# Kernel optimization log

Measured on AMD Instinct MI355X. Metric: run time of the kernel, lower is better.

Reference implementation:

```python
import jax, jax.numpy as jnp
import numpy as np

N_NODES = 20000
N_EDGES = 320000
N_GRAPHS = 64
D = 128  # node_dim


def _gat_conv(h, W, al, ar, b, src, dst, n, res=None, act=None):
    # DGL GATConv: fc -> per-head attn logits -> leaky_relu -> edge softmax per dst -> scatter-add
    H, Dh = al.shape
    feat = (h @ W).reshape(n, H, Dh)                      # [N,H,D]
    el = jnp.einsum('nhd,hd->nh', feat, al)               # [N,H]
    er = jnp.einsum('nhd,hd->nh', feat, ar)               # [N,H]
    e = jax.nn.leaky_relu(el[src] + er[dst], 0.2)         # [E,H]
    m = jax.ops.segment_max(e, dst, num_segments=n)       # [N,H]
    m = jnp.where(jnp.isfinite(m), m, 0.0)
    a = jnp.exp(e - m[dst])                               # [E,H]
    den = jax.ops.segment_sum(a, dst, num_segments=n)     # [N,H]
    a = a / jnp.maximum(den, 1e-9)[dst]
    out = jax.ops.segment_sum(a[:, :, None] * feat[src], dst, num_segments=n)  # [N,H,D]
    if res is not None:
        out = out + res
    out = out + b.reshape(1, H, Dh)
    return act(out) if act is not None else out


def setup_inputs() -> dict:
    key = jax.random.key(0)
    ks = jax.random.split(key, 20)
    s = 0.05
    inp = {
        'h': jax.random.normal(ks[0], (N_NODES, D), jnp.float32),
        'he': jax.random.normal(ks[1], (N_EDGES, 64), jnp.float32),
        'src': jax.random.randint(ks[2], (N_EDGES,), 0, N_NODES),
        'dst': jax.random.randint(ks[3], (N_EDGES,), 0, N_NODES),
        'graph_id': jnp.sort(jax.random.randint(ks[4], (N_NODES,), 0, N_GRAPHS)),
        # layer 0: in=D, heads=4, out=D
        'W0': jax.random.normal(ks[5], (D, 4 * D), jnp.float32) * s,
        'al0': jax.random.normal(ks[6], (4, D), jnp.float32) * s,
        'ar0': jax.random.normal(ks[7], (4, D), jnp.float32) * s,
        'b0': jnp.zeros((4 * D,), jnp.float32),
        # layer 1: in=4D, heads=4, out=D, residual (identity since 4D==4*D)
        'W1': jax.random.normal(ks[8], (4 * D, 4 * D), jnp.float32) * s,
        'al1': jax.random.normal(ks[9], (4, D), jnp.float32) * s,
        'ar1': jax.random.normal(ks[10], (4, D), jnp.float32) * s,
        'b1': jnp.zeros((4 * D,), jnp.float32),
        # layer 2: in=4D, heads=6, out=D, residual via res_fc (4D -> 6D)
        'W2': jax.random.normal(ks[11], (4 * D, 6 * D), jnp.float32) * s,
        'al2': jax.random.normal(ks[12], (6, D), jnp.float32) * s,
        'ar2': jax.random.normal(ks[13], (6, D), jnp.float32) * s,
        'b2': jnp.zeros((6 * D,), jnp.float32),
        'resW2': jax.random.normal(ks[14], (4 * D, 6 * D), jnp.float32) * s,
        # final MLP (1 layer): Linear(D, D)
        'Wm': jax.random.normal(ks[15], (D, D), jnp.float32) * s,
        'bm': jnp.zeros((D,), jnp.float32),
    }
    return inp


def reference(h, he, src, dst, graph_id, W0, al0, ar0, b0, W1, al1, ar1, b1,
              W2, al2, ar2, b2, resW2, Wm, bm):
    n = h.shape[0]
    elu = jax.nn.elu
    # layer 0 (no residual, elu), flatten heads
    x = _gat_conv(h, W0, al0, ar0, b0, src, dst, n, res=None, act=elu)
    x = x.reshape(n, -1)  # [N, 4D]
    # layer 1 (identity residual, elu), flatten heads
    res1 = x.reshape(n, 4, D)
    x2 = _gat_conv(x, W1, al1, ar1, b1, src, dst, n, res=res1, act=elu)
    x2 = x2.reshape(n, -1)  # [N, 4D]
    # layer 2 (linear residual, no activation), mean over heads
    res2 = (x2 @ resW2).reshape(n, 6, D)
    x3 = _gat_conv(x2, W2, al2, ar2, b2, src, dst, n, res=res2, act=None)
    local_feat = x3.mean(axis=1)  # [N, D]
    # avg pooling per graph + linear
    sums = jax.ops.segment_sum(local_feat, graph_id, num_segments=N_GRAPHS)
    cnts = jax.ops.segment_sum(jnp.ones((n,), local_feat.dtype), graph_id, num_segments=N_GRAPHS)
    pooled = sums / jnp.maximum(cnts, 1.0)[:, None]  # [G, D]
    global_feat = pooled @ Wm + bm
    return (local_feat, global_feat)
```

## Files before the change

### kernel.cpp

```cpp
#include <hip/hip_runtime.h>
#include <math.h>


typedef _Float16 f16;
typedef __attribute__((ext_vector_type(8))) _Float16 half8;
typedef __attribute__((ext_vector_type(4))) _Float16 half4;
typedef __attribute__((ext_vector_type(4))) float float4v;

union U16 { unsigned short u; _Float16 h; };

#define M_PAD 20096
#define CHSTRIDE ((size_t)M_PAD * 64)

__device__ inline void gload_lds16(const void* g, void* l) {
    __builtin_amdgcn_global_load_lds((const __attribute__((address_space(1))) unsigned*)g,
                                     (__attribute__((address_space(3))) unsigned*)l,
                                     16, 0, 0);
}


__global__ __launch_bounds__(256) void deg_kernel(const int* __restrict__ dst,
                                                  int* __restrict__ deg, int E) {
    int e = blockIdx.x * 256 + threadIdx.x;
    if (e < E) atomicAdd(&deg[dst[e]], 1);
}

__global__ __launch_bounds__(1024) void scan_kernel(const int* __restrict__ deg,
                                                    int* __restrict__ row_off,
                                                    const int* __restrict__ gid,
                                                    int* __restrict__ gstart, int n) {
    __shared__ int sums[1024];
    int t = threadIdx.x;
    if (t <= 64) {
        int g = t, lo = 0, hi = n;
        while (lo < hi) {
            int mid = (lo + hi) >> 1;
            if (gid[mid] < g) lo = mid + 1; else hi = mid;
        }
        gstart[g] = lo;
    }
    int CH = (n + 1023) >> 10;
    int base = t * CH;
    int s = 0;
    for (int i = 0; i < CH; ++i) { int idx = base + i; if (idx < n) s += deg[idx]; }
    sums[t] = s;
    __syncthreads();
    for (int off = 1; off < 1024; off <<= 1) {
        int v = (t >= off) ? sums[t - off] : 0;
        __syncthreads();
        sums[t] += v;
        __syncthreads();
    }
    int run = (t == 0) ? 0 : sums[t - 1];
    for (int i = 0; i < CH; ++i) {
        int idx = base + i;
        if (idx < n) { row_off[idx] = run; run += deg[idx]; }
    }
    if (t == 1023) row_off[n] = run;
}

__global__ __launch_bounds__(256) void fill_kernel(const int* __restrict__ src,
                                                   const int* __restrict__ dst,
                                                   const int* __restrict__ row_off,
                                                   int* __restrict__ fill,
                                                   int* __restrict__ csr_src, int E) {
    int e = blockIdx.x * 256 + threadIdx.x;
    if (e < E) {
        int d = dst[e];
        int pos = row_off[d] + atomicAdd(&fill[d], 1);
        csr_src[pos] = src[e];
    }
}


__global__ __launch_bounds__(256) void cvt_pad_kernel(const float* __restrict__ x,
                                                      f16* __restrict__ y,
                                                      long n_valid, long n_total) {
    long i = ((long)blockIdx.x * 256 + threadIdx.x) * 4;
    if (i >= n_total) return;
    float4 v = make_float4(0.f, 0.f, 0.f, 0.f);
    if (i < n_valid) v = *(const float4*)&x[i];
    half4 o; o[0] = (f16)v.x; o[1] = (f16)v.y; o[2] = (f16)v.z; o[3] = (f16)v.w;
    *(half4*)&y[i] = o;
}

__global__ __launch_bounds__(256) void zero_pad_kernel(f16* __restrict__ x1,
                                                       f16* __restrict__ x2, int n) {
    int total = (M_PAD - n) * 512;
    int idx = (blockIdx.x * 256 + threadIdx.x) * 4;
    if (idx < total) {
        half4 z; z[0] = (f16)0.f; z[1] = (f16)0.f; z[2] = (f16)0.f; z[3] = (f16)0.f;
        *(half4*)&x1[(size_t)n * 512 + idx] = z;
        *(half4*)&x2[(size_t)n * 512 + idx] = z;
    }
}

__global__ __launch_bounds__(256) void transpose_cvt_kernel(const float* __restrict__ W,
                                                            f16* __restrict__ Wt,
                                                            int K, int N) {
    __shared__ float tile[32][33];
    int n0 = blockIdx.x * 32, k0 = blockIdx.y * 32;
    int tx = threadIdx.x, ty = threadIdx.y;
#pragma unroll
    for (int i = 0; i < 32; i += 8)
        tile[ty + i][tx] = W[(size_t)(k0 + ty + i) * N + n0 + tx];
    __syncthreads();
#pragma unroll
    for (int i = 0; i < 32; i += 8)
        Wt[(size_t)(n0 + ty + i) * K + k0 + tx] = (f16)tile[tx][ty + i];
}


#define STAGE(buf, k0) do {                                   \
    f16* a_ = As + (buf) * 4096 + t * 8;                      \
    f16* b_ = Bs + (buf) * 4096 + t * 8;                      \
    gload_lds16(ag0 + (k0), a_);                              \
    gload_lds16(ag1 + (k0), a_ + 2048);                       \
    gload_lds16(bg0 + (k0), b_);                              \
    gload_lds16(bg1 + (k0), b_ + 2048);                       \
} while (0)

__global__ __launch_bounds__(256) void gemm16_kernel(const f16* __restrict__ A,
                                                     const f16* __restrict__ Bt,
                                                     f16* __restrict__ Cc,
                                                     f16* __restrict__ Cr,
                                                     const float* __restrict__ al,
                                                     const float* __restrict__ ar,
                                                     float* __restrict__ el8,
                                                     float* __restrict__ er8,
                                                     int N, int K, int nchunk,
                                                     int nheads, int nvalid) {
    __shared__ f16 As[2 * 128 * 32];
    __shared__ f16 Bs[2 * 128 * 32];
    __shared__ float elds[2][2][128];
    int t = threadIdx.x;
    int w = t >> 6;
    int l = t & 63;

    int gx = gridDim.x;
    int nwg = gx * gridDim.y;
    int wg = blockIdx.y * gx + blockIdx.x;
    int qq = nwg >> 3, rr = nwg & 7;
    int xcd = wg & 7, idx = wg >> 3;
    int swz = (xcd < rr ? xcd * (qq + 1) : rr * (qq + 1) + (xcd - rr) * qq) + idx;
    int bxi = swz % gx;
    int byi = swz / gx;

    size_t bm = (size_t)byi * 128;
    int bn = bxi * 128;
    int wm = (w & 1) * 64;
    int wn = (w >> 1) * 64;

    int srow = t >> 2;
    int sq = (t & 3) ^ ((srow >> 1) & 3);
    const f16* ag0 = A + (bm + srow) * K + sq * 8;
    const f16* ag1 = A + (bm + 64 + srow) * K + sq * 8;
    const f16* bg0 = Bt + (size_t)(bn + srow) * K + sq * 8;
    const f16* bg1 = Bt + (size_t)(bn + 64 + srow) * K + sq * 8;

    float4v acc[4][4];
#pragma unroll
    for (int i = 0; i < 4; ++i)
#pragma unroll
        for (int j = 0; j < 4; ++j) acc[i][j] = (float4v)(0.f);

    int ml = l & 15, q = l >> 4;
    int sslot = (q ^ ((ml >> 1) & 3)) * 8;
    int apoff = (wm + ml) * 32 + sslot;
    int bpoff = (wn + ml) * 32 + sslot;

    STAGE(0, 0);
    __syncthreads();
    int cur = 0;
    for (int k0 = 0; k0 < K; k0 += 32) {
        if (k0 + 32 < K) STAGE(cur ^ 1, k0 + 32);
        const f16* ap = As + cur * 4096 + apoff;
        const f16* bp = Bs + cur * 4096 + bpoff;
        half8 af[4], bf[4];
#pragma unroll
        for (int mt = 0; mt < 4; ++mt) af[mt] = *(const half8*)(ap + mt * 16 * 32);
#pragma unroll
        for (int nt = 0; nt < 4; ++nt) bf[nt] = *(const half8*)(bp + nt * 16 * 32);
#pragma unroll
        for (int mt = 0; mt < 4; ++mt)
#pragma unroll
            for (int nt = 0; nt < 4; ++nt)
                acc[mt][nt] = __builtin_amdgcn_mfma_f32_16x16x32_f16(bf[nt], af[mt],
                                                                     acc[mt][nt], 0, 0, 0);
        __syncthreads();
        cur ^= 1;
    }
#pragma unroll
    for (int mt = 0; mt < 4; ++mt) {
        size_t row = bm + wm + mt * 16 + ml;
#pragma unroll
        for (int nt = 0; nt < 4; ++nt) {
            half4 hv;
#pragma unroll
            for (int r = 0; r < 4; ++r) hv[r] = (f16)acc[mt][nt][r];
            int col = bn + wn + nt * 16 + q * 4;
            if (col < nchunk) {
                *(half4*)&Cc[(size_t)(col >> 6) * CHSTRIDE + row * 64 + (col & 63)] = hv;
            } else {
                *(half4*)&Cr[row * (size_t)(N - nchunk) + (col - nchunk)] = hv;
            }
        }
    }
    if (al != nullptr && bn < nheads * 128) {
        int hh = bn >> 7;
        float4 a4[4], r4[4];
#pragma unroll
        for (int nt = 0; nt < 4; ++nt) {
            int ci = hh * 128 + wn + nt * 16 + q * 4;
            a4[nt] = *(const float4*)&al[ci];
            r4[nt] = *(const float4*)&ar[ci];
        }
        int wnidx = wn >> 6;
#pragma unroll
        for (int mt = 0; mt < 4; ++mt) {
            float ep = 0.f, rp = 0.f;
#pragma unroll
            for (int nt = 0; nt < 4; ++nt) {
                ep += acc[mt][nt][0] * a4[nt].x + acc[mt][nt][1] * a4[nt].y
                    + acc[mt][nt][2] * a4[nt].z + acc[mt][nt][3] * a4[nt].w;
                rp += acc[mt][nt][0] * r4[nt].x + acc[mt][nt][1] * r4[nt].y
                    + acc[mt][nt][2] * r4[nt].z + acc[mt][nt][3] * r4[nt].w;
            }
            ep += __shfl_xor(ep, 16, 64); ep += __shfl_xor(ep, 32, 64);
            rp += __shfl_xor(rp, 16, 64); rp += __shfl_xor(rp, 32, 64);
            if (q == 0) {
                elds[0][wnidx][wm + mt * 16 + ml] = ep;
                elds[1][wnidx][wm + mt * 16 + ml] = rp;
            }
        }
        __syncthreads();
        int row = t & 127, which = t >> 7;
        long gv = (long)bm + row;
        if (gv < nvalid) {
            float vs = elds[which][0][row] + elds[which][1][row];
            if (which == 0) el8[gv * 8 + hh] = vs;
            else            er8[gv * 8 + hh] = vs;
        }
    }
}


__global__ __launch_bounds__(256, 8) void edge_weight_kernel(
        const float* __restrict__ el8, const float* __restrict__ er8,
        const int* __restrict__ row_off, const int* __restrict__ csr_src,
        unsigned short* __restrict__ wexp, float* __restrict__ inv8,
        int H, int n, int E) {
    int wid = threadIdx.x >> 6, lane = threadIdx.x & 63;
    int c2 = lane >> 4;
    int sl = lane & 15;
    int v = blockIdx.x * 16 + wid * 4 + c2;
    if (v >= n) return;
    float era[6];
    {
        float4 a = *(const float4*)&er8[(size_t)v * 8];
        float2 b = *(const float2*)&er8[(size_t)v * 8 + 4];
        era[0] = a.x; era[1] = a.y; era[2] = a.z; era[3] = a.w;
        era[4] = b.x; era[5] = b.y;
    }
    int beg = row_off[v], end = row_off[v + 1];
    float lsum[6] = {0.f, 0.f, 0.f, 0.f, 0.f, 0.f};
    for (int pos = beg; pos < end; pos += 16) {
        int cnt = min(16, end - pos);
        int s_l = (sl < cnt) ? csr_src[pos + sl] : 0;
        float4 a = *(const float4*)&el8[(size_t)s_l * 8];
        float2 bq = *(const float2*)&el8[(size_t)s_l * 8 + 4];
        float ee[6] = {a.x, a.y, a.z, a.w, bq.x, bq.y};
#pragma unroll
        for (int h = 0; h < 6; ++h) {
            if (h < H) {
                float lg = ee[h] + era[h];
                lg = (lg >= 0.f) ? lg : 0.2f * lg;
                float wv = __expf(lg);
                if (sl >= cnt) wv = 0.f;
                lsum[h] += wv;
                if (sl < cnt) {
                    U16 uu; uu.h = (f16)wv;
                    wexp[(size_t)h * E + pos + sl] = uu.u;
                }
            }
        }
    }
#pragma unroll
    for (int h = 0; h < 6; ++h)
#pragma unroll
        for (int off = 8; off >= 1; off >>= 1)
            lsum[h] += __shfl_xor(lsum[h], off, 64);
    if (sl == 0) {
#pragma unroll
        for (int h = 0; h < 6; ++h)
            if (h < H) inv8[(size_t)v * 8 + h] = 1.f / fmaxf(lsum[h], 1e-9f);
    }
}


__device__ __forceinline__ void agg_chunk_body(
        const f16* __restrict__ fc, const unsigned short* __restrict__ wh,
        const float* __restrict__ inv8, int head,
        const int* __restrict__ row_off, const int* __restrict__ csr_src,
        const f16* __restrict__ res, const float* __restrict__ bias,
        f16* __restrict__ out16, float* __restrict__ out32,
        int n, int width, int act, int chunk,
        int wave_id, int wavestride, int lane) {
    int c = lane >> 3;
    int j = lane & 7;
    int coff = j * 8;
    int cb = chunk * 64 + coff;
    float4 bv0 = *(const float4*)&bias[cb];
    float4 bv1 = *(const float4*)&bias[cb + 4];
    int clbase = lane & 56;

    for (int v0 = wave_id * 8; v0 < n; v0 += wavestride * 8) {
        int v = v0 + c;
        bool valid = (v < n);
        int beg = 0, end = 0;
        if (valid) { beg = row_off[v]; end = row_off[v + 1]; }
        int rounds = end - beg;
        rounds = max(rounds, __shfl_xor(rounds, 8, 64));
        rounds = max(rounds, __shfl_xor(rounds, 16, 64));
        rounds = max(rounds, __shfl_xor(rounds, 32, 64));
        float acc[8] = {0.f, 0.f, 0.f, 0.f, 0.f, 0.f, 0.f, 0.f};
        int s_pf = 0, w_pf = 0;
        for (int r = 0; r < rounds; ++r) {
            if ((r & 7) == 0) {
                int pidx = beg + r + j;
                bool ok = pidx < end;
                s_pf = ok ? csr_src[pidx] : 0;
                w_pf = ok ? (int)wh[pidx] : 0;
            }
            int srcl = clbase + (r & 7);
            int s  = __shfl(s_pf, srcl, 64);
            int wi = __shfl(w_pf, srcl, 64);
            U16 uu; uu.u = (unsigned short)wi;
            float wv = (float)uu.h;
            half8 f = *(const half8*)&fc[(size_t)s * 64 + coff];
#pragma unroll
            for (int k = 0; k < 8; ++k) acc[k] += wv * (float)f[k];
        }
        if (valid) {
            float inv = inv8[(size_t)v * 8 + head];
            float ox[8];
#pragma unroll
            for (int k = 0; k < 8; ++k) ox[k] = acc[k] * inv;
            size_t base = (size_t)v * width + cb;
            if (res) {
                half8 rr = *(const half8*)&res[base];
#pragma unroll
                for (int k = 0; k < 8; ++k) ox[k] += (float)rr[k];
            }
            ox[0] += bv0.x; ox[1] += bv0.y; ox[2] += bv0.z; ox[3] += bv0.w;
            ox[4] += bv1.x; ox[5] += bv1.y; ox[6] += bv1.z; ox[7] += bv1.w;
            if (act) {
#pragma unroll
                for (int k = 0; k < 8; ++k)
                    ox[k] = (ox[k] > 0.f) ? ox[k] : expm1f(ox[k]);
            }
            if (out16) {
                half8 o;
#pragma unroll
                for (int k = 0; k < 8; ++k) o[k] = (f16)ox[k];
                *(half8*)&out16[base] = o;
            } else {
                *(float4*)&out32[base]     = make_float4(ox[0], ox[1], ox[2], ox[3]);
                *(float4*)&out32[base + 4] = make_float4(ox[4], ox[5], ox[6], ox[7]);
            }
        }
    }
}

__global__ __launch_bounds__(256, 8) void agg_chunk_kernel(
        const f16* __restrict__ featc, const unsigned short* __restrict__ wexp,
        const float* __restrict__ inv8,
        const int* __restrict__ row_off, const int* __restrict__ csr_src,
        const f16* __restrict__ res, const float* __restrict__ bias,
        f16* __restrict__ out16, float* __restrict__ out32,
        int n, int nchunks, int width, int E, int act) {
    int wid = threadIdx.x >> 6, lane = threadIdx.x & 63;
    int b = blockIdx.x;
    {
        int chunk = b & 7;
        agg_chunk_body(featc + (size_t)chunk * CHSTRIDE, wexp + (size_t)(chunk >> 1) * E,
                       inv8, chunk >> 1, row_off, csr_src, res, bias, out16, out32,
                       n, width, act, chunk, (b >> 3) * 4 + wid, 1024, lane);
    }
    if (nchunks > 8) {
        int chunk = 8 + (b & 3);
        if (chunk < nchunks)
            agg_chunk_body(featc + (size_t)chunk * CHSTRIDE, wexp + (size_t)(chunk >> 1) * E,
                           inv8, chunk >> 1, row_off, csr_src, res, bias, out16, out32,
                           n, width, act, chunk, (b >> 2) * 4 + wid, 2048, lane);
    }
}


__global__ __launch_bounds__(128) void mean_pool_kernel(const float* __restrict__ x3,
                                                        float* __restrict__ local, int n) {
    int v = blockIdx.x;
    int d = threadIdx.x;
    const float* p = x3 + (size_t)v * 768;
    float s = 0.f;
#pragma unroll
    for (int h = 0; h < 6; ++h) s += p[h * 128 + d];
    local[(size_t)v * 128 + d] = s * (1.f / 6.f);
}

__global__ __launch_bounds__(256) void graph_pool_kernel(const float* __restrict__ local,
                                                         const int* __restrict__ gstart,
                                                         float* __restrict__ pooled) {
    __shared__ float buf[128];
    int g = blockIdx.x;
    int t = threadIdx.x;
    int c = t & 127;
    int sub = t >> 7;
    int beg = gstart[g], end = gstart[g + 1];
    float s = 0.f;
    for (int v = beg + sub; v < end; v += 2) s += local[(size_t)v * 128 + c];
    if (sub == 1) buf[c] = s;
    __syncthreads();
    if (sub == 0) {
        float tot = s + buf[c];
        float cntf = fmaxf((float)(end - beg), 1.f);
        pooled[g * 128 + c] = tot / cntf;
    }
}

__global__ void final_mlp_kernel(const float* __restrict__ pooled,
                                 const float* __restrict__ Wm,
                                 const float* __restrict__ bm,
                                 float* __restrict__ gout) {
    int g = blockIdx.x;
    int j = threadIdx.x;
    __shared__ float p[128];
    p[j] = pooled[g * 128 + j];
    __syncthreads();
    float s = 0.f;
#pragma unroll 16
    for (int k = 0; k < 128; ++k) s += p[k] * Wm[k * 128 + j];
    gout[g * 128 + j] = s + bm[j];
}


extern "C" void kernel_launch(void* const* d_in, const int* in_sizes, int n_in,
                              void* d_out, int out_size, void* d_ws, size_t ws_size,
                              hipStream_t stream) {
    const float* h     = (const float*)d_in[0];
    const int*   src   = (const int*)d_in[2];
    const int*   dst   = (const int*)d_in[3];
    const int*   gid   = (const int*)d_in[4];
    const float* W0    = (const float*)d_in[5];
    const float* al0   = (const float*)d_in[6];
    const float* ar0   = (const float*)d_in[7];
    const float* b0    = (const float*)d_in[8];
    const float* W1    = (const float*)d_in[9];
    const float* al1   = (const float*)d_in[10];
    const float* ar1   = (const float*)d_in[11];
    const float* b1    = (const float*)d_in[12];
    const float* W2    = (const float*)d_in[13];
    const float* al2   = (const float*)d_in[14];
    const float* ar2   = (const float*)d_in[15];
    const float* b2    = (const float*)d_in[16];
    const float* resW2 = (const float*)d_in[17];
    const float* Wm    = (const float*)d_in[18];
    const float* bm    = (const float*)d_in[19];

    const int n = in_sizes[0] / 128;
    const int E = in_sizes[2];

    size_t off = 0;
    auto take = [&](size_t bytes) -> void* {
        void* p = (char*)d_ws + off;
        off = (off + bytes + 255) & ~(size_t)255;
        return p;
    };
    f16* h16     = (f16*)take((size_t)M_PAD * 128 * 2);
    f16* Wt0     = (f16*)take((size_t)512 * 128 * 2);
    f16* Wt1     = (f16*)take((size_t)512 * 512 * 2);
    f16* Wt2cat  = (f16*)take((size_t)1536 * 512 * 2);
    f16* featc   = (f16*)take((size_t)12 * CHSTRIDE * 2);
    f16* res2    = (f16*)take((size_t)M_PAD * 768 * 2);
    f16* x1_16   = (f16*)take((size_t)M_PAD * 512 * 2);
    f16* x2_16   = (f16*)take((size_t)M_PAD * 512 * 2);
    float* x3    = (float*)take((size_t)n * 768 * 4);
    unsigned short* wexp = (unsigned short*)take((size_t)6 * E * 2);
    float* inv8  = (float*)take((size_t)n * 8 * 4);
    float* el8   = (float*)take((size_t)n * 8 * 4);
    float* er8   = (float*)take((size_t)n * 8 * 4);
    int* deg     = (int*)take((size_t)2 * n * 4);
    int* fillc   = deg + n;
    int* row_off = (int*)take((size_t)(n + 1) * 4);
    int* csr_src = (int*)take((size_t)E * 4);
    int* gstart  = (int*)take(65 * 4);
    float* pooled = (float*)take(64 * 128 * 4);

    float* out_local  = (float*)d_out;
    float* out_global = (float*)d_out + (size_t)n * 128;

    hipMemsetAsync(deg, 0, (size_t)2 * n * 4, stream);
    zero_pad_kernel<<<(int)(((size_t)(M_PAD - n) * 512 / 4 + 255) / 256), 256, 0, stream>>>(x1_16, x2_16, n);

    {
        long nv = (long)n * 128, nt = (long)M_PAD * 128;
        cvt_pad_kernel<<<(int)((nt / 4 + 255) / 256), 256, 0, stream>>>(h, h16, nv, nt);
    }
    transpose_cvt_kernel<<<dim3(512 / 32, 128 / 32), dim3(32, 8), 0, stream>>>(W0, Wt0, 128, 512);
    transpose_cvt_kernel<<<dim3(512 / 32, 512 / 32), dim3(32, 8), 0, stream>>>(W1, Wt1, 512, 512);
    transpose_cvt_kernel<<<dim3(768 / 32, 512 / 32), dim3(32, 8), 0, stream>>>(W2, Wt2cat, 512, 768);
    transpose_cvt_kernel<<<dim3(768 / 32, 512 / 32), dim3(32, 8), 0, stream>>>(resW2, Wt2cat + (size_t)768 * 512, 512, 768);

    deg_kernel<<<(E + 255) / 256, 256, 0, stream>>>(dst, deg, E);
    scan_kernel<<<1, 1024, 0, stream>>>(deg, row_off, gid, gstart, n);
    fill_kernel<<<(E + 255) / 256, 256, 0, stream>>>(src, dst, row_off, fillc, csr_src, E);

    const int gy = M_PAD / 128;
    const int ew_blocks = (n + 15) / 16;

    gemm16_kernel<<<dim3(512 / 128, gy), 256, 0, stream>>>(h16, Wt0, featc, nullptr,
                                                           al0, ar0, el8, er8, 512, 128, 512, 4, n);
    edge_weight_kernel<<<ew_blocks, 256, 0, stream>>>(el8, er8, row_off, csr_src, wexp, inv8, 4, n, E);
    agg_chunk_kernel<<<2048, 256, 0, stream>>>(featc, wexp, inv8, row_off, csr_src,
                                               nullptr, b0, x1_16, nullptr, n, 8, 512, E, 1);
    gemm16_kernel<<<dim3(512 / 128, gy), 256, 0, stream>>>(x1_16, Wt1, featc, nullptr,
                                                           al1, ar1, el8, er8, 512, 512, 512, 4, n);
    edge_weight_kernel<<<ew_blocks, 256, 0, stream>>>(el8, er8, row_off, csr_src, wexp, inv8, 4, n, E);
    agg_chunk_kernel<<<2048, 256, 0, stream>>>(featc, wexp, inv8, row_off, csr_src,
                                               x1_16, b1, x2_16, nullptr, n, 8, 512, E, 1);
    gemm16_kernel<<<dim3(1536 / 128, gy), 256, 0, stream>>>(x2_16, Wt2cat, featc, res2,
                                                            al2, ar2, el8, er8, 1536, 512, 768, 6, n);
    edge_weight_kernel<<<ew_blocks, 256, 0, stream>>>(el8, er8, row_off, csr_src, wexp, inv8, 6, n, E);
    agg_chunk_kernel<<<2048, 256, 0, stream>>>(featc, wexp, inv8, row_off, csr_src,
                                               res2, b2, nullptr, x3, n, 12, 768, E, 0);
    mean_pool_kernel<<<n, 128, 0, stream>>>(x3, out_local, n);
    graph_pool_kernel<<<64, 256, 0, stream>>>(out_local, gstart, pooled);
    final_mlp_kernel<<<64, 128, 0, stream>>>(pooled, Wm, bm, out_global);
}
```

Measured before the change: 555.5 us.

## Pack src index with fp16 weight, batch gathers, fuse head-mean and pooling

The edge-weight kernel now writes a packed 32-bit word holding the source index (low 16 bits) and the fp16 attention weight (high 16 bits), so aggregation reads one stream instead of two. The aggregation loop issues eight feature gathers per round with the next packed words prefetched, aiming to raise memory-level parallelism; launch bounds drop to 5 waves per SIMD to fit the extra registers. The last layer adds the head mean straight into the output with float atomics, which removes the x3 buffer and the mean kernel, and graph pooling is fused with the final linear layer. The risks are atomic contention plus a non-deterministic summation order, and the 16-bit index packing, which only holds while the node count stays below 65536.

```diff
diff --git a/kernel.cpp b/kernel.cpp
--- a/kernel.cpp
+++ b/kernel.cpp
@@ -248,7 +248,7 @@
 __global__ __launch_bounds__(256, 8) void edge_weight_kernel(
         const float* __restrict__ el8, const float* __restrict__ er8,
         const int* __restrict__ row_off, const int* __restrict__ csr_src,
-        unsigned short* __restrict__ wexp, float* __restrict__ inv8,
+        int* __restrict__ wp, float* __restrict__ inv8,
         int H, int n, int E) {
     int wid = threadIdx.x >> 6, lane = threadIdx.x & 63;
     int c2 = lane >> 4;
@@ -280,7 +280,7 @@
                 lsum[h] += wv;
                 if (sl < cnt) {
                     U16 uu; uu.h = (f16)wv;
-                    wexp[(size_t)h * E + pos + sl] = uu.u;
+                    wp[(size_t)h * E + pos + sl] = s_l | ((int)uu.u << 16);
                 }
             }
         }
@@ -299,12 +299,12 @@
 
 
 __device__ __forceinline__ void agg_chunk_body(
-        const f16* __restrict__ fc, const unsigned short* __restrict__ wh,
+        const f16* __restrict__ fc, const int* __restrict__ wp,
         const float* __restrict__ inv8, int head,
-        const int* __restrict__ row_off, const int* __restrict__ csr_src,
+        const int* __restrict__ row_off,
         const f16* __restrict__ res, const float* __restrict__ bias,
         f16* __restrict__ out16, float* __restrict__ out32,
-        int n, int width, int act, int chunk,
+        int n, int width, int act, int domean, int chunk,
         int wave_id, int wavestride, int lane) {
     int c = lane >> 3;
     int j = lane & 7;
@@ -324,22 +324,26 @@
         rounds = max(rounds, __shfl_xor(rounds, 16, 64));
         rounds = max(rounds, __shfl_xor(rounds, 32, 64));
         float acc[8] = {0.f, 0.f, 0.f, 0.f, 0.f, 0.f, 0.f, 0.f};
-        int s_pf = 0, w_pf = 0;
-        for (int r = 0; r < rounds; ++r) {
-            if ((r & 7) == 0) {
-                int pidx = beg + r + j;
-                bool ok = pidx < end;
-                s_pf = ok ? csr_src[pidx] : 0;
-                w_pf = ok ? (int)wh[pidx] : 0;
-            }
-            int srcl = clbase + (r & 7);
-            int s  = __shfl(s_pf, srcl, 64);
-            int wi = __shfl(w_pf, srcl, 64);
-            U16 uu; uu.u = (unsigned short)wi;
-            float wv = (float)uu.h;
-            half8 f = *(const half8*)&fc[(size_t)s * 64 + coff];
-#pragma unroll
-            for (int k = 0; k < 8; ++k) acc[k] += wv * (float)f[k];
+        int pidx = beg + j;
+        int pk = (pidx < end) ? wp[pidx] : 0;
+        for (int base = 0; base < rounds; base += 8) {
+            int pn = beg + base + 8 + j;
+            int pk_nxt = (pn < end) ? wp[pn] : 0;
+            int pe[8];
+#pragma unroll
+            for (int e = 0; e < 8; ++e) pe[e] = __shfl(pk, clbase + e, 64);
+            half8 f[8];
+#pragma unroll
+            for (int e = 0; e < 8; ++e)
+                f[e] = *(const half8*)&fc[(size_t)(pe[e] & 0xFFFF) * 64 + coff];
+#pragma unroll
+            for (int e = 0; e < 8; ++e) {
+                U16 uu; uu.u = (unsigned short)((unsigned)pe[e] >> 16);
+                float wv = (float)uu.h;
+#pragma unroll
+                for (int k = 0; k < 8; ++k) acc[k] += wv * (float)f[e][k];
+            }
+            pk = pk_nxt;
         }
         if (valid) {
             float inv = inv8[(size_t)v * 8 + head];
@@ -359,7 +363,11 @@
                 for (int k = 0; k < 8; ++k)
                     ox[k] = (ox[k] > 0.f) ? ox[k] : expm1f(ox[k]);
             }
-            if (out16) {
+            if (domean) {
+                float* dst = out32 + (size_t)v * 128 + (cb & 127);
+#pragma unroll
+                for (int k = 0; k < 8; ++k) atomicAdd(&dst[k], ox[k] * (1.f / 6.f));
+            } else if (out16) {
                 half8 o;
 #pragma unroll
                 for (int k = 0; k < 8; ++k) o[k] = (f16)ox[k];
@@ -372,75 +380,61 @@
     }
 }
 
-__global__ __launch_bounds__(256, 8) void agg_chunk_kernel(
-        const f16* __restrict__ featc, const unsigned short* __restrict__ wexp,
+__global__ __launch_bounds__(256, 5) void agg_chunk_kernel(
+        const f16* __restrict__ featc, const int* __restrict__ wp,
         const float* __restrict__ inv8,
-        const int* __restrict__ row_off, const int* __restrict__ csr_src,
+        const int* __restrict__ row_off,
         const f16* __restrict__ res, const float* __restrict__ bias,
         f16* __restrict__ out16, float* __restrict__ out32,
-        int n, int nchunks, int width, int E, int act) {
+        int n, int nchunks, int width, int E, int act, int domean) {
     int wid = threadIdx.x >> 6, lane = threadIdx.x & 63;
     int b = blockIdx.x;
     {
         int chunk = b & 7;
-        agg_chunk_body(featc + (size_t)chunk * CHSTRIDE, wexp + (size_t)(chunk >> 1) * E,
-                       inv8, chunk >> 1, row_off, csr_src, res, bias, out16, out32,
-                       n, width, act, chunk, (b >> 3) * 4 + wid, 1024, lane);
+        agg_chunk_body(featc + (size_t)chunk * CHSTRIDE, wp + (size_t)(chunk >> 1) * E,
+                       inv8, chunk >> 1, row_off, res, bias, out16, out32,
+                       n, width, act, domean, chunk, (b >> 3) * 4 + wid, 1024, lane);
     }
     if (nchunks > 8) {
         int chunk = 8 + (b & 3);
         if (chunk < nchunks)
-            agg_chunk_body(featc + (size_t)chunk * CHSTRIDE, wexp + (size_t)(chunk >> 1) * E,
-                           inv8, chunk >> 1, row_off, csr_src, res, bias, out16, out32,
-                           n, width, act, chunk, (b >> 2) * 4 + wid, 2048, lane);
-    }
-}
-
-
-__global__ __launch_bounds__(128) void mean_pool_kernel(const float* __restrict__ x3,
-                                                        float* __restrict__ local, int n) {
-    int v = blockIdx.x;
-    int d = threadIdx.x;
-    const float* p = x3 + (size_t)v * 768;
-    float s = 0.f;
-#pragma unroll
-    for (int h = 0; h < 6; ++h) s += p[h * 128 + d];
-    local[(size_t)v * 128 + d] = s * (1.f / 6.f);
-}
-
-__global__ __launch_bounds__(256) void graph_pool_kernel(const float* __restrict__ local,
-                                                         const int* __restrict__ gstart,
-                                                         float* __restrict__ pooled) {
-    __shared__ float buf[128];
+            agg_chunk_body(featc + (size_t)chunk * CHSTRIDE, wp + (size_t)(chunk >> 1) * E,
+                           inv8, chunk >> 1, row_off, res, bias, out16, out32,
+                           n, width, act, domean, chunk, (b >> 2) * 4 + wid, 2048, lane);
+    }
+}
+
+
+__global__ __launch_bounds__(1024) void graph_pool_kernel(const float* __restrict__ local,
+                                                          const int* __restrict__ gstart,
+                                                          const float* __restrict__ Wm,
+                                                          const float* __restrict__ bm,
+                                                          float* __restrict__ gout) {
+    __shared__ float buf[8][128];
+    __shared__ float p[128];
     int g = blockIdx.x;
     int t = threadIdx.x;
     int c = t & 127;
     int sub = t >> 7;
     int beg = gstart[g], end = gstart[g + 1];
     float s = 0.f;
-    for (int v = beg + sub; v < end; v += 2) s += local[(size_t)v * 128 + c];
-    if (sub == 1) buf[c] = s;
+    for (int v = beg + sub; v < end; v += 8) s += local[(size_t)v * 128 + c];
+    buf[sub][c] = s;
     __syncthreads();
     if (sub == 0) {
-        float tot = s + buf[c];
+        float tot = 0.f;
+#pragma unroll
+        for (int k = 0; k < 8; ++k) tot += buf[k][c];
         float cntf = fmaxf((float)(end - beg), 1.f);
-        pooled[g * 128 + c] = tot / cntf;
-    }
-}
-
-__global__ void final_mlp_kernel(const float* __restrict__ pooled,
-                                 const float* __restrict__ Wm,
-                                 const float* __restrict__ bm,
-                                 float* __restrict__ gout) {
-    int g = blockIdx.x;
-    int j = threadIdx.x;
-    __shared__ float p[128];
-    p[j] = pooled[g * 128 + j];
+        p[c] = tot / cntf;
+    }
     __syncthreads();
-    float s = 0.f;
+    if (t < 128) {
+        float s2 = 0.f;
 #pragma unroll 16
-    for (int k = 0; k < 128; ++k) s += p[k] * Wm[k * 128 + j];
-    gout[g * 128 + j] = s + bm[j];
+        for (int k = 0; k < 128; ++k) s2 += p[k] * Wm[k * 128 + t];
+        gout[g * 128 + t] = s2 + bm[t];
+    }
 }
 
 
@@ -484,8 +478,7 @@
     f16* res2    = (f16*)take((size_t)M_PAD * 768 * 2);
     f16* x1_16   = (f16*)take((size_t)M_PAD * 512 * 2);
     f16* x2_16   = (f16*)take((size_t)M_PAD * 512 * 2);
-    float* x3    = (float*)take((size_t)n * 768 * 4);
-    unsigned short* wexp = (unsigned short*)take((size_t)6 * E * 2);
+    int* wp      = (int*)take((size_t)6 * E * 4);
     float* inv8  = (float*)take((size_t)n * 8 * 4);
     float* el8   = (float*)take((size_t)n * 8 * 4);
     float* er8   = (float*)take((size_t)n * 8 * 4);
@@ -494,12 +487,12 @@
     int* row_off = (int*)take((size_t)(n + 1) * 4);
     int* csr_src = (int*)take((size_t)E * 4);
     int* gstart  = (int*)take(65 * 4);
-    float* pooled = (float*)take(64 * 128 * 4);
 
     float* out_local  = (float*)d_out;
     float* out_global = (float*)d_out + (size_t)n * 128;
 
     hipMemsetAsync(deg, 0, (size_t)2 * n * 4, stream);
+    hipMemsetAsync(out_local, 0, (size_t)n * 128 * 4, stream);
     zero_pad_kernel<<<(int)(((size_t)(M_PAD - n) * 512 / 4 + 255) / 256), 256, 0, stream>>>(x1_16, x2_16, n);
 
     {
@@ -520,20 +513,18 @@
 
     gemm16_kernel<<<dim3(512 / 128, gy), 256, 0, stream>>>(h16, Wt0, featc, nullptr,
                                                            al0, ar0, el8, er8, 512, 128, 512, 4, n);
-    edge_weight_kernel<<<ew_blocks, 256, 0, stream>>>(el8, er8, row_off, csr_src, wexp, inv8, 4, n, E);
-    agg_chunk_kernel<<<2048, 256, 0, stream>>>(featc, wexp, inv8, row_off, csr_src,
-                                               nullptr, b0, x1_16, nullptr, n, 8, 512, E, 1);
+    edge_weight_kernel<<<ew_blocks, 256, 0, stream>>>(el8, er8, row_off, csr_src, wp, inv8, 4, n, E);
+    agg_chunk_kernel<<<2048, 256, 0, stream>>>(featc, wp, inv8, row_off,
+                                               nullptr, b0, x1_16, nullptr, n, 8, 512, E, 1, 0);
     gemm16_kernel<<<dim3(512 / 128, gy), 256, 0, stream>>>(x1_16, Wt1, featc, nullptr,
                                                            al1, ar1, el8, er8, 512, 512, 512, 4, n);
-    edge_weight_kernel<<<ew_blocks, 256, 0, stream>>>(el8, er8, row_off, csr_src, wexp, inv8, 4, n, E);
-    agg_chunk_kernel<<<2048, 256, 0, stream>>>(featc, wexp, inv8, row_off, csr_src,
-                                               x1_16, b1, x2_16, nullptr, n, 8, 512, E, 1);
+    edge_weight_kernel<<<ew_blocks, 256, 0, stream>>>(el8, er8, row_off, csr_src, wp, inv8, 4, n, E);
+    agg_chunk_kernel<<<2048, 256, 0, stream>>>(featc, wp, inv8, row_off,
+                                               x1_16, b1, x2_16, nullptr, n, 8, 512, E, 1, 0);
     gemm16_kernel<<<dim3(1536 / 128, gy), 256, 0, stream>>>(x2_16, Wt2cat, featc, res2,
                                                             al2, ar2, el8, er8, 1536, 512, 768, 6, n);
-    edge_weight_kernel<<<ew_blocks, 256, 0, stream>>>(el8, er8, row_off, csr_src, wexp, inv8, 6, n, E);
-    agg_chunk_kernel<<<2048, 256, 0, stream>>>(featc, wexp, inv8, row_off, csr_src,
-                                               res2, b2, nullptr, x3, n, 12, 768, E, 0);
-    mean_pool_kernel<<<n, 128, 0, stream>>>(x3, out_local, n);
-    graph_pool_kernel<<<64, 256, 0, stream>>>(out_local, gstart, pooled);
-    final_mlp_kernel<<<64, 128, 0, stream>>>(pooled, Wm, bm, out_global);
-}
+    edge_weight_kernel<<<ew_blocks, 256, 0, stream>>>(el8, er8, row_off, csr_src, wp, inv8, 6, n, E);
+    agg_chunk_kernel<<<2048, 256, 0, stream>>>(featc, wp, inv8, row_off,
+                                               res2, b2, nullptr, out_local, n, 12, 768, E, 0, 1);
+    graph_pool_kernel<<<64, 1024, 0, stream>>>(out_local, gstart, Wm, bm, out_global);
+}
```

Result: slower. 876.2 us (+57.7%).
